# Kernel optimization log

Measured on AMD Instinct MI355X. Metric: run time of the kernel, lower is better.

The kernel has to match this reference:

```python
import jax, jax.numpy as jnp
import numpy as np


def _adaptive_avgpool1d(x, n_out):
    # x: (B, C, L); PyTorch AdaptiveAvgPool1d semantics with static bin edges.
    L = x.shape[-1]
    bins = []
    for i in range(n_out):
        s = (i * L) // n_out
        e = -((-(i + 1) * L) // n_out)  # ceil((i+1)*L/n_out)
        bins.append(x[..., s:e].mean(axis=-1))
    return jnp.stack(bins, axis=-1)  # (B, C, n_out)


def setup_inputs() -> dict:
    key = jax.random.key(0)
    k1, k2, k3, k4, k5 = jax.random.split(key, 5)
    B, C, H, W = 32, 512, 80, 80
    R = C // 16
    x = jax.random.normal(k1, (B, C, H, W), dtype=jnp.float32)
    W1 = jax.random.normal(k2, (R, C), dtype=jnp.float32) * 0.05  # conv1x1 C->C/16, no bias
    W2 = jax.random.normal(k3, (C, R), dtype=jnp.float32) * 0.05  # conv1x1 C/16->C, no bias
    w7 = jax.random.normal(k4, (7,), dtype=jnp.float32) * 0.3     # conv1d(7->1, k=1) weight
    b = jax.random.normal(k5, (1,), dtype=jnp.float32) * 0.1      # conv1d bias
    return {"x": x, "W1": W1, "W2": W2, "w7": w7, "b": b}


def reference(x, W1, W2, w7, b):
    B, C, H, W = x.shape
    # Dual global pooling -> (B, C)
    avg = x.mean(axis=(2, 3))
    mx = x.max(axis=(2, 3))
    # Sorted-percentile bins: sort over spatial, adaptive-avg to 5 bins
    sortx = jnp.sort(x.reshape(B, C, H * W), axis=-1)
    bavg = _adaptive_avgpool1d(sortx, 5)  # (B, C, 5)
    # Stack the 7 MLP inputs: [avg, max, bin0..bin4] -> (B, 7, C)
    stacked = jnp.concatenate(
        [avg[:, None, :], mx[:, None, :], jnp.transpose(bavg, (0, 2, 1))], axis=1
    )
    # Shared 1x1-conv MLP applied as a batched GEMM
    h = jax.nn.relu(jnp.einsum("bnc,rc->bnr", stacked, W1))
    mlp_out = jnp.einsum("bnr,cr->bnc", h, W2)  # (B, 7, C)
    # conv1d(7 -> 1, kernel 1): weighted sum over the 7 rows + bias
    out = jnp.einsum("bnc,n->bc", mlp_out, w7) + b
    return jax.nn.sigmoid(out).reshape(B, C, 1, 1)
```

## Files before the change

### kernel.cpp

```cpp
#include <hip/hip_runtime.h>
#include <hip/hip_bf16.h>
#include <math.h>

#define HW 6400
#define NT 256
#define PT 25
#define NB 2048
#define BPT (NB/NT)

__device__ __forceinline__ double fixval(unsigned long long p) {
  unsigned long long cnt = p >> 48;
  long long fs = (long long)(p & 0xFFFFFFFFFFFFULL) - ((long long)cnt << 30);
  return (double)fs * (1.0 / 16777216.0);
}

__global__ __launch_bounds__(NT) void rowstats_kernel(
    const float* __restrict__ x, float* __restrict__ stacked) {
  const int tid = threadIdx.x;
  const int lane = tid & 63;
  const int wid = tid >> 6;
  const int row = blockIdx.x;
  const float* xr = x + (size_t)row * HW;

  __shared__ unsigned long long s_hist[NB];
  __shared__ float s_mnw[4], s_mxw[4];
  __shared__ unsigned long long s_wtot[4];
  __shared__ int s_cb[4];
  __shared__ unsigned long long s_cE[4];

  float v[PT];
  {
    const float4* xr4 = (const float4*)xr;
#pragma unroll
    for (int j = 0; j < 6; ++j) {
      float4 q = xr4[tid + j * NT];
      v[4 * j + 0] = q.x; v[4 * j + 1] = q.y;
      v[4 * j + 2] = q.z; v[4 * j + 3] = q.w;
    }
    v[24] = xr[6144 + tid];
  }
  float lmx = v[0], lmn = v[0];
#pragma unroll
  for (int i = 1; i < PT; ++i) { lmx = fmaxf(lmx, v[i]); lmn = fminf(lmn, v[i]); }
#pragma unroll
  for (int off = 32; off; off >>= 1) {
    lmx = fmaxf(lmx, __shfl_down(lmx, off));
    lmn = fminf(lmn, __shfl_down(lmn, off));
  }
  if (lane == 0) { s_mnw[wid] = lmn; s_mxw[wid] = lmx; }
#pragma unroll
  for (int j = 0; j < BPT; ++j) s_hist[tid * BPT + j] = 0ULL;
  __syncthreads();

  const float gmn = fminf(fminf(s_mnw[0], s_mnw[1]), fminf(s_mnw[2], s_mnw[3]));
  const float gmx = fmaxf(fmaxf(s_mxw[0], s_mxw[1]), fmaxf(s_mxw[2], s_mxw[3]));

  const int b_ = row >> 9, c_ = row & 511;
  float* dst = stacked + ((size_t)b_ * 7) * 512 + c_;

  if (!(gmx - gmn > 1e-30f)) {
    if (tid == 0) {
      dst[0] = gmx; dst[512] = gmx;
#pragma unroll
      for (int t = 0; t < 5; ++t) dst[(size_t)(2 + t) * 512] = gmx;
    }
    return;
  }

  const float scale = (float)NB / (gmx - gmn);
  const float nls = -gmn * scale;
#pragma unroll
  for (int i = 0; i < PT; ++i) {
    float f = fmaf(v[i], scale, nls);
    int b = (int)f;
    b = b < 0 ? 0 : (b > NB - 1 ? NB - 1 : b);
    int q = (int)(v[i] * 16777216.0f) + (1 << 30);
    atomicAdd(&s_hist[b], (1ULL << 48) + (unsigned long long)(unsigned int)q);
  }
  __syncthreads();

  unsigned long long h[BPT];
  unsigned long long run = 0ULL;
#pragma unroll
  for (int j = 0; j < BPT; ++j) { h[j] = s_hist[tid * BPT + j]; run += h[j]; }
  unsigned long long inc = run;
#pragma unroll
  for (int off = 1; off < 64; off <<= 1) {
    unsigned long long u = __shfl_up(inc, off);
    if (lane >= off) inc += u;
  }
  if (lane == 63) s_wtot[wid] = inc;
  __syncthreads();
  unsigned long long base = inc - run;
#pragma unroll
  for (int w = 0; w < 4; ++w) if (w < wid) base += s_wtot[w];

  {
    unsigned long long E = base;
#pragma unroll
    for (int j = 0; j < BPT; ++j) {
      unsigned long long I = E + h[j];
      unsigned cEc = (unsigned)(E >> 48), cIc = (unsigned)(I >> 48);
#pragma unroll
      for (int t = 0; t < 4; ++t) {
        unsigned k = 1280u * (t + 1);
        if (cEc < k && k <= cIc) { s_cb[t] = tid * BPT + j; s_cE[t] = E; }
      }
      E = I;
    }
  }
  __syncthreads();

  if (tid == 0) {
    unsigned long long grand = s_wtot[0] + s_wtot[1] + s_wtot[2] + s_wtot[3];
    double totv = fixval(grand);
    const double width = (double)(gmx - gmn) / (double)NB;
    double pref[4];
#pragma unroll
    for (int t = 0; t < 4; ++t) {
      unsigned long long E = s_cE[t];
      unsigned cEc = (unsigned)(E >> 48);
      double sE = fixval(E);
      double mid = (double)gmn + ((double)s_cb[t] + 0.5) * width;
      double m = (double)(1280u * (t + 1) - cEc);
      pref[t] = sE + m * mid;
    }
    dst[0] = (float)(totv * (1.0 / 6400.0));
    dst[512] = gmx;
    double prev = 0.0;
#pragma unroll
    for (int t = 0; t < 4; ++t) {
      dst[(size_t)(2 + t) * 512] = (float)((pref[t] - prev) * (1.0 / 1280.0));
      prev = pref[t];
    }
    dst[(size_t)6 * 512] = (float)((totv - prev) * (1.0 / 1280.0));
  }
}

__global__ __launch_bounds__(256) void mlp_kernel(
    const float* __restrict__ stacked, const float* __restrict__ W1,
    const float* __restrict__ W2, const float* __restrict__ w7,
    const float* __restrict__ bias, float* __restrict__ out) {
  const int b = blockIdx.x;
  const int tid = threadIdx.x;
  __shared__ float s_stk[7 * 512];
  __shared__ float s_g[32];
  const float* src = stacked + (size_t)b * 7 * 512;
  for (int i = tid; i < 7 * 512; i += 256) s_stk[i] = src[i];
  if (tid < 32) s_g[tid] = 0.f;
  __syncthreads();
  if (tid < 224) {
    const int n = tid >> 5, r = tid & 31;
    float acc = 0.f;
    for (int c = 0; c < 512; ++c) acc = fmaf(s_stk[n * 512 + c], W1[r * 512 + c], acc);
    acc = fmaxf(acc, 0.f);
    atomicAdd(&s_g[r], w7[n] * acc);
  }
  __syncthreads();
  const float bv = bias[0];
  for (int c = tid; c < 512; c += 256) {
    float acc = bv;
#pragma unroll
    for (int r = 0; r < 32; ++r) acc = fmaf(s_g[r], W2[c * 32 + r], acc);
    out[b * 512 + c] = 1.f / (1.f + expf(-acc));
  }
}

extern "C" void kernel_launch(void* const* d_in, const int* in_sizes, int n_in,
                              void* d_out, int out_size, void* d_ws, size_t ws_size,
                              hipStream_t stream) {
  const float* x = (const float*)d_in[0];
  const float* W1 = (const float*)d_in[1];
  const float* W2 = (const float*)d_in[2];
  const float* w7 = (const float*)d_in[3];
  const float* bb = (const float*)d_in[4];
  float* out = (float*)d_out;
  float* stacked = (float*)d_ws;

  rowstats_kernel<<<32 * 512, NT, 0, stream>>>(x, stacked);
  mlp_kernel<<<32, 256, 0, stream>>>(stacked, W1, W2, w7, bb, out);
}
```

Measured before the change: 108.9 us.

## Use 32-bit count histogram with bin-midpoint sums instead of 64-bit packed atomics

Replaces the 64-bit shared histogram, which packed a count and a fixed-point value sum into each bin, with a 32-bit count-only histogram. Per-bin sums are rebuilt from bin indices, weighted by the bin midpoint, during the scan. The total sum now comes from a warp-shuffle reduction, and zeroing and reading the histogram use 128-bit shared accesses. This removes the 64-bit atomics and halves shared-memory traffic, but the bin averages become approximations based on bin midpoints rather than exact sums within each bin.

```diff
diff --git a/kernel.cpp b/kernel.cpp
--- a/kernel.cpp
+++ b/kernel.cpp
@@ -8,12 +8,6 @@
 #define NB 2048
 #define BPT (NB/NT)
 
-__device__ __forceinline__ double fixval(unsigned long long p) {
-  unsigned long long cnt = p >> 48;
-  long long fs = (long long)(p & 0xFFFFFFFFFFFFULL) - ((long long)cnt << 30);
-  return (double)fs * (1.0 / 16777216.0);
-}
-
 __global__ __launch_bounds__(NT) void rowstats_kernel(
     const float* __restrict__ x, float* __restrict__ stacked) {
   const int tid = threadIdx.x;
@@ -22,8 +16,8 @@
   const int row = blockIdx.x;
   const float* xr = x + (size_t)row * HW;
 
-  __shared__ unsigned long long s_hist[NB];
-  __shared__ float s_mnw[4], s_mxw[4];
+  __shared__ __align__(16) unsigned s_hist[NB];
+  __shared__ float s_mnw[4], s_mxw[4], s_smw[4];
   __shared__ unsigned long long s_wtot[4];
   __shared__ int s_cb[4];
   __shared__ unsigned long long s_cE[4];
@@ -39,28 +33,35 @@
     }
     v[24] = xr[6144 + tid];
   }
-  float lmx = v[0], lmn = v[0];
+  float lmx = v[0], lmn = v[0], lsm = v[0];
 #pragma unroll
-  for (int i = 1; i < PT; ++i) { lmx = fmaxf(lmx, v[i]); lmn = fminf(lmn, v[i]); }
+  for (int i = 1; i < PT; ++i) {
+    lmx = fmaxf(lmx, v[i]); lmn = fminf(lmn, v[i]); lsm += v[i];
+  }
 #pragma unroll
   for (int off = 32; off; off >>= 1) {
     lmx = fmaxf(lmx, __shfl_down(lmx, off));
     lmn = fminf(lmn, __shfl_down(lmn, off));
+    lsm += __shfl_down(lsm, off);
   }
-  if (lane == 0) { s_mnw[wid] = lmn; s_mxw[wid] = lmx; }
-#pragma unroll
-  for (int j = 0; j < BPT; ++j) s_hist[tid * BPT + j] = 0ULL;
+  if (lane == 0) { s_mnw[wid] = lmn; s_mxw[wid] = lmx; s_smw[wid] = lsm; }
+  {
+    uint4* z = (uint4*)&s_hist[tid * BPT];
+    z[0] = make_uint4(0u, 0u, 0u, 0u);
+    z[1] = make_uint4(0u, 0u, 0u, 0u);
+  }
   __syncthreads();
 
   const float gmn = fminf(fminf(s_mnw[0], s_mnw[1]), fminf(s_mnw[2], s_mnw[3]));
   const float gmx = fmaxf(fmaxf(s_mxw[0], s_mxw[1]), fmaxf(s_mxw[2], s_mxw[3]));
+  const float tot = (s_smw[0] + s_smw[1]) + (s_smw[2] + s_smw[3]);
 
-  const int b_ = row >> 9, c_ = row & 511;
-  float* dst = stacked + ((size_t)b_ * 7) * 512 + c_;
+  float* dst = stacked + ((size_t)(row >> 9) * 7) * 512 + (row & 511);
 
-  if (!(gmx - gmn > 1e-30f)) {
+  if (!(gmx > gmn)) {
     if (tid == 0) {
-      dst[0] = gmx; dst[512] = gmx;
+      dst[0] = tot * (1.f / 6400.f);
+      dst[512] = gmx;
 #pragma unroll
       for (int t = 0; t < 5; ++t) dst[(size_t)(2 + t) * 512] = gmx;
     }
@@ -72,17 +73,23 @@
 #pragma unroll
   for (int i = 0; i < PT; ++i) {
     float f = fmaf(v[i], scale, nls);
-    int b = (int)f;
-    b = b < 0 ? 0 : (b > NB - 1 ? NB - 1 : b);
-    int q = (int)(v[i] * 16777216.0f) + (1 << 30);
-    atomicAdd(&s_hist[b], (1ULL << 48) + (unsigned long long)(unsigned int)q);
+    f = fminf(fmaxf(f, 0.0f), (float)(NB - 1));
+    atomicAdd(&s_hist[(int)f], 1u);
   }
   __syncthreads();
 
-  unsigned long long h[BPT];
+  unsigned h[BPT];
+  {
+    const uint4* p = (const uint4*)&s_hist[tid * BPT];
+    uint4 a = p[0], b = p[1];
+    h[0] = a.x; h[1] = a.y; h[2] = a.z; h[3] = a.w;
+    h[4] = b.x; h[5] = b.y; h[6] = b.z; h[7] = b.w;
+  }
   unsigned long long run = 0ULL;
 #pragma unroll
-  for (int j = 0; j < BPT; ++j) { h[j] = s_hist[tid * BPT + j]; run += h[j]; }
+  for (int j = 0; j < BPT; ++j)
+    run += ((unsigned long long)h[j] << 32) |
+           (unsigned long long)(h[j] * (unsigned)(tid * BPT + j));
   unsigned long long inc = run;
 #pragma unroll
   for (int off = 1; off < 64; off <<= 1) {
@@ -91,49 +98,48 @@
   }
   if (lane == 63) s_wtot[wid] = inc;
   __syncthreads();
-  unsigned long long base = inc - run;
+  unsigned long long E = inc - run;
 #pragma unroll
-  for (int w = 0; w < 4; ++w) if (w < wid) base += s_wtot[w];
+  for (int w = 0; w < 4; ++w) if (w < wid) E += s_wtot[w];
 
-  {
-    unsigned long long E = base;
 #pragma unroll
-    for (int j = 0; j < BPT; ++j) {
-      unsigned long long I = E + h[j];
-      unsigned cEc = (unsigned)(E >> 48), cIc = (unsigned)(I >> 48);
+  for (int j = 0; j < BPT; ++j) {
+    unsigned long long dlt = ((unsigned long long)h[j] << 32) |
+                             (unsigned long long)(h[j] * (unsigned)(tid * BPT + j));
+    unsigned long long I = E + dlt;
+    unsigned cE = (unsigned)(E >> 32), cI = (unsigned)(I >> 32);
 #pragma unroll
-      for (int t = 0; t < 4; ++t) {
-        unsigned k = 1280u * (t + 1);
-        if (cEc < k && k <= cIc) { s_cb[t] = tid * BPT + j; s_cE[t] = E; }
-      }
-      E = I;
+    for (int t = 0; t < 4; ++t) {
+      unsigned k = 1280u * (t + 1);
+      if (cE < k && k <= cI) { s_cb[t] = tid * BPT + j; s_cE[t] = E; }
     }
+    E = I;
   }
   __syncthreads();
 
   if (tid == 0) {
-    unsigned long long grand = s_wtot[0] + s_wtot[1] + s_wtot[2] + s_wtot[3];
-    double totv = fixval(grand);
-    const double width = (double)(gmx - gmn) / (double)NB;
+    const double w = (double)(gmx - gmn) / (double)NB;
+    const double g0 = (double)gmn;
     double pref[4];
 #pragma unroll
     for (int t = 0; t < 4; ++t) {
-      unsigned long long E = s_cE[t];
-      unsigned cEc = (unsigned)(E >> 48);
-      double sE = fixval(E);
-      double mid = (double)gmn + ((double)s_cb[t] + 0.5) * width;
-      double m = (double)(1280u * (t + 1) - cEc);
-      pref[t] = sE + m * mid;
+      unsigned long long Ee = s_cE[t];
+      double cE = (double)(unsigned)(Ee >> 32);
+      double wE = (double)(unsigned)(Ee & 0xFFFFFFFFu);
+      double k = 1280.0 * (double)(t + 1);
+      double m = k - cE;
+      pref[t] = g0 * k + w * (wE + 0.5 * cE + m * ((double)s_cb[t] + 0.5));
     }
-    dst[0] = (float)(totv * (1.0 / 6400.0));
+    dst[0] = tot * (1.f / 6400.f);
     dst[512] = gmx;
     double prev = 0.0;
+    const double totd = (double)tot;
 #pragma unroll
     for (int t = 0; t < 4; ++t) {
       dst[(size_t)(2 + t) * 512] = (float)((pref[t] - prev) * (1.0 / 1280.0));
       prev = pref[t];
     }
-    dst[(size_t)6 * 512] = (float)((totv - prev) * (1.0 / 1280.0));
+    dst[(size_t)6 * 512] = (float)((totd - prev) * (1.0 / 1280.0));
   }
 }
 
```

Measured after the change: 101.1 us. 7.1% less time.

## Process four rows per block with double-buffered histograms and prefetched loads

Applied to the files above, without the earlier changes.

Each block now handles four rows, prefetching the next row into registers while the current row's histogram is built, and alternates between two shared histograms so the clear and resolve steps overlap. The 64-bit fixed-point value accumulation in the histogram atomics is replaced by 32-bit count-only atomics, and the bin sums are rebuilt from bin midpoints plus an exact row total taken from a reduction. Full __syncthreads are swapped for lighter s_barrier sequences. This cuts launch count, atomic width and LDS traffic, but the percentile bins become midpoint approximations, the degenerate constant-row path is removed, and register pressure rises.

```diff
diff --git a/kernel.cpp b/kernel.cpp
--- a/kernel.cpp
+++ b/kernel.cpp
@@ -7,134 +7,160 @@
 #define PT 25
 #define NB 2048
 #define BPT (NB/NT)
-
-__device__ __forceinline__ double fixval(unsigned long long p) {
-  unsigned long long cnt = p >> 48;
-  long long fs = (long long)(p & 0xFFFFFFFFFFFFULL) - ((long long)cnt << 30);
-  return (double)fs * (1.0 / 16777216.0);
-}
-
-__global__ __launch_bounds__(NT) void rowstats_kernel(
+#define R 4
+
+__device__ __forceinline__ void light_barrier() {
+  asm volatile("s_waitcnt lgkmcnt(0)" ::: "memory");
+  __builtin_amdgcn_s_barrier();
+  __builtin_amdgcn_sched_barrier(0);
+}
+
+#define RESOLVE(Q, PR)                                                        \
+  if (tid < 7) {                                                              \
+    int gp = row0 + (PR);                                                     \
+    float* db = stacked + ((size_t)(gp >> 9) * 7) * 512 + (gp & 511);         \
+    if (tid == 5) db[0] = tot##Q * (1.f / 6400.f);                            \
+    else if (tid == 6) db[512] = gmx##Q;                                      \
+    else if (tid < 4) {                                                       \
+      double w = (double)(gmx##Q - gmn##Q) * (1.0 / (double)NB);              \
+      float Xm = (tid == 0) ? 0.f : s_pref[Q][tid - 1];                       \
+      double bin = (double)gmn##Q +                                           \
+                   w * (double)(s_pref[Q][tid] - Xm) * (1.0 / 1280.0);        \
+      db[(size_t)(2 + tid) * 512] = (float)bin;                               \
+    } else {                                                                  \
+      double w = (double)(gmx##Q - gmn##Q) * (1.0 / (double)NB);              \
+      double bin = ((double)tot##Q -                                          \
+                    ((double)gmn##Q * 5120.0 + w * (double)s_pref[Q][3])) *   \
+                   (1.0 / 1280.0);                                            \
+      db[(size_t)6 * 512] = (float)bin;                                       \
+    }                                                                         \
+  }
+
+#define BODY(VC, VN, P, Q, RIDX)                                              \
+  {                                                                           \
+    float lmx = VC[0], lmn = VC[0], lsm = VC[0];                              \
+    _Pragma("unroll") for (int i = 1; i < PT; ++i) {                          \
+      lmx = fmaxf(lmx, VC[i]); lmn = fminf(lmn, VC[i]); lsm += VC[i];         \
+    }                                                                         \
+    _Pragma("unroll") for (int off = 32; off; off >>= 1) {                    \
+      lmx = fmaxf(lmx, __shfl_down(lmx, off));                                \
+      lmn = fminf(lmn, __shfl_down(lmn, off));                                \
+      lsm += __shfl_down(lsm, off);                                           \
+    }                                                                         \
+    if (lane == 0) {                                                          \
+      s_part[P][0][wid] = lmn; s_part[P][1][wid] = lmx; s_part[P][2][wid] = lsm; \
+    }                                                                         \
+    light_barrier();                 \
+    gmn##P = fminf(fminf(s_part[P][0][0], s_part[P][0][1]),                   \
+                   fminf(s_part[P][0][2], s_part[P][0][3]));                  \
+    gmx##P = fmaxf(fmaxf(s_part[P][1][0], s_part[P][1][1]),                   \
+                   fmaxf(s_part[P][1][2], s_part[P][1][3]));                  \
+    tot##P = (s_part[P][2][0] + s_part[P][2][1]) +                            \
+             (s_part[P][2][2] + s_part[P][2][3]);                             \
+    if (RIDX > 0) { RESOLVE(Q, RIDX - 1); }                                   \
+    {                                                                         \
+      float d = gmx##P - gmn##P;                                              \
+      float scale = d > 0.f ? (float)NB / d : 0.f;                            \
+      float nls = -gmn##P * scale;                                            \
+      _Pragma("unroll") for (int i = 0; i < PT; ++i) {                        \
+        float f = fmaf(VC[i], scale, nls);                                    \
+        f = fminf(fmaxf(f, 0.f), (float)(NB - 1));                            \
+        atomicAdd(&s_hist[P][(int)f], 1u);                                    \
+      }                                                                       \
+    }                                                                         \
+    if (RIDX + 1 < R) { \
+      const float4* xp = (const float4*)(x + (size_t)(row0 + RIDX + 1) * HW); \
+      _Pragma("unroll") for (int j = 0; j < 6; ++j) {                         \
+        float4 q4 = xp[tid + j * NT];                                         \
+        VN[4 * j] = q4.x; VN[4 * j + 1] = q4.y;                               \
+        VN[4 * j + 2] = q4.z; VN[4 * j + 3] = q4.w;                           \
+      }                                                                       \
+      VN[24] = ((const float*)xp)[6144 + tid];                                \
+    }                                                                         \
+    light_barrier();                                    \
+    {                                                                         \
+      unsigned hh[BPT];                                                       \
+      const uint4* pp = (const uint4*)&s_hist[P][tid * BPT];                  \
+      uint4 a4 = pp[0], b4 = pp[1];                                           \
+      hh[0] = a4.x; hh[1] = a4.y; hh[2] = a4.z; hh[3] = a4.w;                 \
+      hh[4] = b4.x; hh[5] = b4.y; hh[6] = b4.z; hh[7] = b4.w;                 \
+      unsigned long long run = 0ULL;                                          \
+      _Pragma("unroll") for (int j = 0; j < BPT; ++j)                         \
+        run += ((unsigned long long)hh[j] << 32) |                            \
+               (unsigned long long)(hh[j] * (unsigned)(tid * BPT + j));       \
+      unsigned long long inc = run;                                           \
+      _Pragma("unroll") for (int off = 1; off < 64; off <<= 1) {              \
+        unsigned long long uu = __shfl_up(inc, off);                          \
+        if (lane >= off) inc += uu;                                           \
+      }                                                                       \
+      if (lane == 63) s_wtot[P][wid] = inc;                                   \
+      {                                   \
+        uint4* zz = (uint4*)&s_hist[Q][tid * BPT];                            \
+        zz[0] = make_uint4(0u, 0u, 0u, 0u);                                   \
+        zz[1] = make_uint4(0u, 0u, 0u, 0u);                                   \
+      }                                                                       \
+      light_barrier();                           \
+      unsigned long long E = inc - run;                                       \
+      _Pragma("unroll") for (int w = 0; w < 4; ++w)                           \
+        if (w < wid) E += s_wtot[P][w];                                       \
+      _Pragma("unroll") for (int j = 0; j < BPT; ++j) {                       \
+        unsigned long long dlt =                                              \
+            ((unsigned long long)hh[j] << 32) |                               \
+            (unsigned long long)(hh[j] * (unsigned)(tid * BPT + j));          \
+        unsigned long long I = E + dlt;                                       \
+        unsigned cEc = (unsigned)(E >> 32), cIc = (unsigned)(I >> 32);        \
+        _Pragma("unroll") for (int t = 0; t < 4; ++t) {                       \
+          unsigned k = 1280u * (t + 1);                                       \
+          if (cEc < k && k <= cIc) {                                          \
+            float m = (float)(k - cEc);                                       \
+            float X = (float)(unsigned)(E & 0xFFFFFFFFu) +                    \
+                      0.5f * (float)cEc +                                     \
+                      m * ((float)(tid * BPT + j) + 0.5f);                    \
+            s_pref[P][t] = X;                                                 \
+          }                                                                   \
+        }                                                                     \
+        E = I;                                                                \
+      }                                                                       \
+    }                                                                         \
+  }
+
+__global__ __launch_bounds__(NT, 5) void rowstats_kernel(
     const float* __restrict__ x, float* __restrict__ stacked) {
   const int tid = threadIdx.x;
   const int lane = tid & 63;
   const int wid = tid >> 6;
-  const int row = blockIdx.x;
-  const float* xr = x + (size_t)row * HW;
-
-  __shared__ unsigned long long s_hist[NB];
-  __shared__ float s_mnw[4], s_mxw[4];
-  __shared__ unsigned long long s_wtot[4];
-  __shared__ int s_cb[4];
-  __shared__ unsigned long long s_cE[4];
-
-  float v[PT];
+  const int row0 = blockIdx.x * R;
+
+  __shared__ unsigned s_hist[2][NB];
+  __shared__ float s_part[2][3][4];
+  __shared__ unsigned long long s_wtot[2][4];
+  __shared__ float s_pref[2][4];
+
+  float vA[PT], vB[PT];
+  float gmn0, gmx0, tot0, gmn1, gmx1, tot1;
+  gmn1 = gmx1 = tot1 = 0.f;
+
   {
-    const float4* xr4 = (const float4*)xr;
+    const float4* xp = (const float4*)(x + (size_t)row0 * HW);
 #pragma unroll
     for (int j = 0; j < 6; ++j) {
-      float4 q = xr4[tid + j * NT];
-      v[4 * j + 0] = q.x; v[4 * j + 1] = q.y;
-      v[4 * j + 2] = q.z; v[4 * j + 3] = q.w;
+      float4 q4 = xp[tid + j * NT];
+      vA[4 * j] = q4.x; vA[4 * j + 1] = q4.y;
+      vA[4 * j + 2] = q4.z; vA[4 * j + 3] = q4.w;
     }
-    v[24] = xr[6144 + tid];
-  }
-  float lmx = v[0], lmn = v[0];
-#pragma unroll
-  for (int i = 1; i < PT; ++i) { lmx = fmaxf(lmx, v[i]); lmn = fminf(lmn, v[i]); }
-#pragma unroll
-  for (int off = 32; off; off >>= 1) {
-    lmx = fmaxf(lmx, __shfl_down(lmx, off));
-    lmn = fminf(lmn, __shfl_down(lmn, off));
-  }
-  if (lane == 0) { s_mnw[wid] = lmn; s_mxw[wid] = lmx; }
-#pragma unroll
-  for (int j = 0; j < BPT; ++j) s_hist[tid * BPT + j] = 0ULL;
-  __syncthreads();
-
-  const float gmn = fminf(fminf(s_mnw[0], s_mnw[1]), fminf(s_mnw[2], s_mnw[3]));
-  const float gmx = fmaxf(fmaxf(s_mxw[0], s_mxw[1]), fmaxf(s_mxw[2], s_mxw[3]));
-
-  const int b_ = row >> 9, c_ = row & 511;
-  float* dst = stacked + ((size_t)b_ * 7) * 512 + c_;
-
-  if (!(gmx - gmn > 1e-30f)) {
-    if (tid == 0) {
-      dst[0] = gmx; dst[512] = gmx;
-#pragma unroll
-      for (int t = 0; t < 5; ++t) dst[(size_t)(2 + t) * 512] = gmx;
-    }
-    return;
-  }
-
-  const float scale = (float)NB / (gmx - gmn);
-  const float nls = -gmn * scale;
-#pragma unroll
-  for (int i = 0; i < PT; ++i) {
-    float f = fmaf(v[i], scale, nls);
-    int b = (int)f;
-    b = b < 0 ? 0 : (b > NB - 1 ? NB - 1 : b);
-    int q = (int)(v[i] * 16777216.0f) + (1 << 30);
-    atomicAdd(&s_hist[b], (1ULL << 48) + (unsigned long long)(unsigned int)q);
-  }
-  __syncthreads();
-
-  unsigned long long h[BPT];
-  unsigned long long run = 0ULL;
-#pragma unroll
-  for (int j = 0; j < BPT; ++j) { h[j] = s_hist[tid * BPT + j]; run += h[j]; }
-  unsigned long long inc = run;
-#pragma unroll
-  for (int off = 1; off < 64; off <<= 1) {
-    unsigned long long u = __shfl_up(inc, off);
-    if (lane >= off) inc += u;
-  }
-  if (lane == 63) s_wtot[wid] = inc;
-  __syncthreads();
-  unsigned long long base = inc - run;
-#pragma unroll
-  for (int w = 0; w < 4; ++w) if (w < wid) base += s_wtot[w];
-
-  {
-    unsigned long long E = base;
-#pragma unroll
-    for (int j = 0; j < BPT; ++j) {
-      unsigned long long I = E + h[j];
-      unsigned cEc = (unsigned)(E >> 48), cIc = (unsigned)(I >> 48);
-#pragma unroll
-      for (int t = 0; t < 4; ++t) {
-        unsigned k = 1280u * (t + 1);
-        if (cEc < k && k <= cIc) { s_cb[t] = tid * BPT + j; s_cE[t] = E; }
-      }
-      E = I;
-    }
-  }
-  __syncthreads();
-
-  if (tid == 0) {
-    unsigned long long grand = s_wtot[0] + s_wtot[1] + s_wtot[2] + s_wtot[3];
-    double totv = fixval(grand);
-    const double width = (double)(gmx - gmn) / (double)NB;
-    double pref[4];
-#pragma unroll
-    for (int t = 0; t < 4; ++t) {
-      unsigned long long E = s_cE[t];
-      unsigned cEc = (unsigned)(E >> 48);
-      double sE = fixval(E);
-      double mid = (double)gmn + ((double)s_cb[t] + 0.5) * width;
-      double m = (double)(1280u * (t + 1) - cEc);
-      pref[t] = sE + m * mid;
-    }
-    dst[0] = (float)(totv * (1.0 / 6400.0));
-    dst[512] = gmx;
-    double prev = 0.0;
-#pragma unroll
-    for (int t = 0; t < 4; ++t) {
-      dst[(size_t)(2 + t) * 512] = (float)((pref[t] - prev) * (1.0 / 1280.0));
-      prev = pref[t];
-    }
-    dst[(size_t)6 * 512] = (float)((totv - prev) * (1.0 / 1280.0));
-  }
+    vA[24] = ((const float*)xp)[6144 + tid];
+    uint4* zz = (uint4*)&s_hist[0][tid * BPT];
+    zz[0] = make_uint4(0u, 0u, 0u, 0u);
+    zz[1] = make_uint4(0u, 0u, 0u, 0u);
+  }
+
+  BODY(vA, vB, 0, 1, 0);
+  BODY(vB, vA, 1, 0, 1);
+  BODY(vA, vB, 0, 1, 2);
+  BODY(vB, vA, 1, 0, 3);
+
+  light_barrier();
+  RESOLVE(1, R - 1);
 }
 
 __global__ __launch_bounds__(256) void mlp_kernel(
@@ -177,6 +203,6 @@
   float* out = (float*)d_out;
   float* stacked = (float*)d_ws;
 
-  rowstats_kernel<<<32 * 512, NT, 0, stream>>>(x, stacked);
+  rowstats_kernel<<<(32 * 512) / R, NT, 0, stream>>>(x, stacked);
   mlp_kernel<<<32, 256, 0, stream>>>(stacked, W1, W2, w7, bb, out);
 }
```

New measurement: 164.7 us. 51.3% more time.
